# Kernel tuning notes

Measured on AMD Instinct MI355X. Metric: run time of the kernel, lower is better.

## Reference

```python
import jax, jax.numpy as jnp
import numpy as np

N_NODES = 100000
N_EDGES = 3200000
IN_CH = 16
HIDDEN = 32
NUM_HH = 1000


def setup_inputs() -> dict:
    key = jax.random.key(0)
    ks = jax.random.split(key, 10)
    x = jax.random.normal(ks[0], (N_NODES, IN_CH), dtype=jnp.float32)
    edge_index = jax.random.randint(ks[1], (2, N_EDGES), 0, N_NODES, dtype=jnp.int64)
    s = 1.0 / np.sqrt(IN_CH)
    w1_l = jax.random.uniform(ks[2], (IN_CH, HIDDEN), jnp.float32, -s, s)
    w1_r = jax.random.uniform(ks[3], (IN_CH, HIDDEN), jnp.float32, -s, s)
    b1 = jnp.zeros((HIDDEN,), jnp.float32)
    s2 = 1.0 / np.sqrt(HIDDEN)
    w2_l = jax.random.uniform(ks[4], (HIDDEN, HIDDEN), jnp.float32, -s2, s2)
    w2_r = jax.random.uniform(ks[5], (HIDDEN, HIDDEN), jnp.float32, -s2, s2)
    b2 = jnp.zeros((HIDDEN,), jnp.float32)
    fc_w = jax.random.uniform(ks[6], (HIDDEN, NUM_HH), jnp.float32, -s2, s2)
    fc_b = jnp.zeros((NUM_HH,), jnp.float32)
    return {"x": x, "edge_index": edge_index, "w1_l": w1_l, "w1_r": w1_r, "b1": b1,
            "w2_l": w2_l, "w2_r": w2_r, "b2": b2, "fc_w": fc_w, "fc_b": fc_b}


def _sage_conv(h, src, dst, w_l, w_r, b, n_nodes):
    # mean-aggregate source features onto targets (PyG SAGEConv, aggr='mean')
    msg = h[src]                                            # [E, F] gather
    agg = jax.ops.segment_sum(msg, dst, num_segments=n_nodes)
    cnt = jax.ops.segment_sum(jnp.ones((src.shape[0], 1), h.dtype), dst,
                              num_segments=n_nodes)
    mean = agg / jnp.maximum(cnt, 1.0)
    # out = lin_l(mean_neighbors) + lin_r(x); bias lives in lin_l
    return mean @ w_l + b + h @ w_r


def reference(x, edge_index, w1_l, w1_r, b1, w2_l, w2_r, b2, fc_w, fc_b):
    src, dst = edge_index[0], edge_index[1]
    n = x.shape[0]
    h = jax.nn.relu(_sage_conv(x, src, dst, w1_l, w1_r, b1, n))
    h = jax.nn.relu(_sage_conv(h, src, dst, w2_l, w2_r, b2, n))
    return h @ fc_w + fc_b
```

## Files before the change

kernel.cpp:

```cpp
#include <hip/hip_runtime.h>

#define N_NODES 100000
#define IN_CH 16
#define HIDDEN 32
#define NUM_HH 1000

#define NPB 128
#define NBUCK ((N_NODES + NPB - 1) / NPB)
#define NCHUNK 512
#define SCAN_N (NBUCK * NCHUNK)
#define S1_BLOCKS ((SCAN_N + 1023) / 1024)
#define SORT_CAP 6144

__global__ __launch_bounds__(256) void passA_count(const int* __restrict__ dst,
                                                   int* __restrict__ counts,
                                                   int n_edges, int cepb) {
  __shared__ int hist[NBUCK];
  for (int i = threadIdx.x; i < NBUCK; i += 256) hist[i] = 0;
  __syncthreads();
  const int s = blockIdx.x * cepb;
  const int e = min(n_edges, s + cepb);
  for (int i = s + threadIdx.x; i < e; i += 256)
    atomicAdd(&hist[dst[i] >> 7], 1);
  __syncthreads();
  for (int i = threadIdx.x; i < NBUCK; i += 256)
    counts[i * NCHUNK + blockIdx.x] = hist[i];
}

__global__ __launch_bounds__(1024) void scan_local(const int* __restrict__ in,
                                                   int* __restrict__ out,
                                                   int* __restrict__ partials) {
  __shared__ int tmp[1024];
  const int i = blockIdx.x * 1024 + threadIdx.x;
  const int v = (i < SCAN_N) ? in[i] : 0;
  tmp[threadIdx.x] = v;
  __syncthreads();
  for (int off = 1; off < 1024; off <<= 1) {
    int t = (threadIdx.x >= off) ? tmp[threadIdx.x - off] : 0;
    __syncthreads();
    tmp[threadIdx.x] += t;
    __syncthreads();
  }
  if (i < SCAN_N) out[i] = tmp[threadIdx.x] - v;
  if (threadIdx.x == 1023) partials[blockIdx.x] = tmp[threadIdx.x];
}

__global__ __launch_bounds__(512) void scan_partials(int* __restrict__ partials) {
  __shared__ int tmp[512];
  const int v = (threadIdx.x < S1_BLOCKS) ? partials[threadIdx.x] : 0;
  tmp[threadIdx.x] = v;
  __syncthreads();
  for (int off = 1; off < 512; off <<= 1) {
    int t = (threadIdx.x >= off) ? tmp[threadIdx.x - off] : 0;
    __syncthreads();
    tmp[threadIdx.x] += t;
    __syncthreads();
  }
  if (threadIdx.x < S1_BLOCKS) partials[threadIdx.x] = tmp[threadIdx.x] - v;
}

__global__ __launch_bounds__(1024) void scan_add(int* __restrict__ out,
                                                 const int* __restrict__ partials,
                                                 int* __restrict__ bucket_ptr,
                                                 int n_edges) {
  const int i = blockIdx.x * 1024 + threadIdx.x;
  if (i < SCAN_N) {
    const int v = out[i] + partials[blockIdx.x];
    out[i] = v;
    if ((i & (NCHUNK - 1)) == 0) bucket_ptr[i / NCHUNK] = v;
  }
  if (i == 0) bucket_ptr[NBUCK] = n_edges;
}

__global__ __launch_bounds__(256) void passB_scatter(
    const int* __restrict__ src, const int* __restrict__ dst,
    const int* __restrict__ offs, unsigned* __restrict__ packed, int n_edges,
    int cepb) {
  __shared__ int cur[NBUCK];
  for (int i = threadIdx.x; i < NBUCK; i += 256)
    cur[i] = offs[i * NCHUNK + blockIdx.x];
  __syncthreads();
  const int s = blockIdx.x * cepb;
  const int e = min(n_edges, s + cepb);
  for (int i = s + threadIdx.x; i < e; i += 256) {
    const int d = dst[i];
    const int b = d >> 7;
    const int pos = atomicAdd(&cur[b], 1);
    packed[pos] = (unsigned)src[i] | ((unsigned)(d & (NPB - 1)) << 17);
  }
}

__global__ __launch_bounds__(512) void bucket_sort(
    unsigned* __restrict__ packed, const int* __restrict__ bucket_ptr,
    int* __restrict__ row_ptr, int n_edges) {
  __shared__ unsigned stage[SORT_CAP];
  __shared__ int bins[NPB];
  __shared__ int scn[NPB];
  __shared__ int cur[NPB];
  const int b = blockIdx.x;
  const int s = bucket_ptr[b];
  const int cnt = bucket_ptr[b + 1] - s;
  const int tid = threadIdx.x;

  if (tid < NPB) bins[tid] = 0;
  __syncthreads();
  for (int i = tid; i < cnt; i += 512) {
    const unsigned pk = packed[s + i];
    stage[i] = pk;
    atomicAdd(&bins[pk >> 17], 1);
  }
  __syncthreads();
  if (tid < NPB) scn[tid] = bins[tid];
  __syncthreads();
  for (int off = 1; off < NPB; off <<= 1) {
    int t = (tid < NPB && tid >= off) ? scn[tid - off] : 0;
    __syncthreads();
    if (tid < NPB) scn[tid] += t;
    __syncthreads();
  }
  if (tid < NPB) {
    const int excl = scn[tid] - bins[tid];
    cur[tid] = excl;
    const int node = b * NPB + tid;
    if (node < N_NODES) row_ptr[node] = s + excl;
  }
  if (b == NBUCK - 1 && tid == 0) row_ptr[N_NODES] = n_edges;
  __syncthreads();
  for (int i = tid; i < cnt; i += 512) {
    const unsigned pk = stage[i];
    const int pos = atomicAdd(&cur[pk >> 17], 1);
    packed[s + pos] = pk & 0x1FFFFu;
  }
}

template <int CH, bool FC>
__global__ __launch_bounds__(512) void sage_block(
    const float* __restrict__ feat, const int* __restrict__ row_ptr,
    const int* __restrict__ adj, const float* __restrict__ w_l,
    const float* __restrict__ w_r, const float* __restrict__ b,
    float* __restrict__ out, const float* __restrict__ fcw,
    const float* __restrict__ fcb) {
  constexpr int Q = CH / 4;
  constexpr int EPW = 64 / Q;
  __shared__ float wl[CH * HIDDEN];
  __shared__ float wr[CH * HIDDEN];
  __shared__ float bs[HIDDEN];
  __shared__ float mean_s[8][CH];
  __shared__ float xs[8][CH];
  __shared__ float hs[FC ? NPB * HIDDEN : 1];

  const int tid = threadIdx.x;
  for (int i = tid; i < CH * HIDDEN; i += 512) {
    wl[i] = w_l[i];
    wr[i] = w_r[i];
  }
  if (tid < HIDDEN) bs[tid] = b[tid];
  __syncthreads();

  const int wave = tid >> 6;
  const int lane = tid & 63;
  const int base = blockIdx.x * NPB;
  const int q = lane & (Q - 1);
  const int esub = lane / Q;
  const int j = lane & 31;
  const int p = lane >> 5;

#pragma unroll 1
  for (int pass = 0; pass < NPB / 8; ++pass) {
    const int l = pass * 8 + wave;
    const int n = base + l;
    if (n < N_NODES) {
      const int s = row_ptr[n];
      const int e = row_ptr[n + 1];

      float4 acc = {0.f, 0.f, 0.f, 0.f};
      for (int i = s + esub; i < e; i += EPW) {
        const float4 v = ((const float4*)(feat + (size_t)adj[i] * CH))[q];
        acc.x += v.x;
        acc.y += v.y;
        acc.z += v.z;
        acc.w += v.w;
      }
#pragma unroll
      for (int m = Q; m < 64; m <<= 1) {
        acc.x += __shfl_xor(acc.x, m, 64);
        acc.y += __shfl_xor(acc.y, m, 64);
        acc.z += __shfl_xor(acc.z, m, 64);
        acc.w += __shfl_xor(acc.w, m, 64);
      }
      const float inv = 1.0f / fmaxf((float)(e - s), 1.0f);
      if (esub == 0) {
        mean_s[wave][4 * q + 0] = acc.x * inv;
        mean_s[wave][4 * q + 1] = acc.y * inv;
        mean_s[wave][4 * q + 2] = acc.z * inv;
        mean_s[wave][4 * q + 3] = acc.w * inv;
        const float4 xv = ((const float4*)(feat + (size_t)n * CH))[q];
        xs[wave][4 * q + 0] = xv.x;
        xs[wave][4 * q + 1] = xv.y;
        xs[wave][4 * q + 2] = xv.z;
        xs[wave][4 * q + 3] = xv.w;
      }
      __builtin_amdgcn_wave_barrier();

      float o = 0.f;
#pragma unroll
      for (int k = p * (CH / 2); k < (p + 1) * (CH / 2); ++k)
        o = fmaf(mean_s[wave][k], wl[k * HIDDEN + j],
                 fmaf(xs[wave][k], wr[k * HIDDEN + j], o));
      o += __shfl_xor(o, 32, 64);
      o = fmaxf(o + bs[j], 0.f);
      if (p == 0) {
        if (FC)
          hs[l * HIDDEN + j] = o;
        else
          out[(size_t)n * HIDDEN + j] = o;
      }
      __builtin_amdgcn_wave_barrier();
    }
  }

  if (FC) {
    __syncthreads();
    const int nvalid = min(NPB, N_NODES - base);
#pragma unroll
    for (int c = 0; c < 2; ++c) {
      const int jj = c * 512 + tid;
      if (jj < NUM_HH) {
        float w[HIDDEN];
#pragma unroll
        for (int k = 0; k < HIDDEN; ++k) w[k] = fcw[k * NUM_HH + jj];
        const float bias = fcb[jj];
        for (int n = 0; n < nvalid; ++n) {
          float a = bias;
#pragma unroll
          for (int k = 0; k < HIDDEN; ++k)
            a = fmaf(hs[n * HIDDEN + k], w[k], a);
          out[(size_t)(base + n) * NUM_HH + jj] = a;
        }
      }
    }
  }
}

extern "C" void kernel_launch(void* const* d_in, const int* in_sizes, int n_in,
                              void* d_out, int out_size, void* d_ws,
                              size_t ws_size, hipStream_t stream) {
  const float* x = (const float*)d_in[0];
  const int* edge = (const int*)d_in[1];
  const float* w1_l = (const float*)d_in[2];
  const float* w1_r = (const float*)d_in[3];
  const float* b1 = (const float*)d_in[4];
  const float* w2_l = (const float*)d_in[5];
  const float* w2_r = (const float*)d_in[6];
  const float* b2 = (const float*)d_in[7];
  const float* fc_w = (const float*)d_in[8];
  const float* fc_b = (const float*)d_in[9];
  float* out = (float*)d_out;

  const int n_edges = in_sizes[1] / 2;
  const int* src = edge;
  const int* dst = edge + n_edges;

  unsigned* packed = (unsigned*)d_ws;
  float* h1 = (float*)(packed + n_edges);
  int* counts = (int*)(h1 + (size_t)N_NODES * HIDDEN);
  int* offs = counts + SCAN_N;
  int* bucket_ptr = offs + SCAN_N;
  int* partials = bucket_ptr + NBUCK + 1;
  int* row_ptr = partials + S1_BLOCKS + 1;

  const int cepb = (n_edges + NCHUNK - 1) / NCHUNK;

  passA_count<<<NCHUNK, 256, 0, stream>>>(dst, counts, n_edges, cepb);
  scan_local<<<S1_BLOCKS, 1024, 0, stream>>>(counts, offs, partials);
  scan_partials<<<1, 512, 0, stream>>>(partials);
  scan_add<<<S1_BLOCKS, 1024, 0, stream>>>(offs, partials, bucket_ptr, n_edges);
  passB_scatter<<<NCHUNK, 256, 0, stream>>>(src, dst, offs, packed, n_edges,
                                            cepb);
  bucket_sort<<<NBUCK, 512, 0, stream>>>(packed, bucket_ptr, row_ptr, n_edges);

  sage_block<IN_CH, false><<<NBUCK, 512, 0, stream>>>(
      x, row_ptr, (const int*)packed, w1_l, w1_r, b1, h1, nullptr, nullptr);
  sage_block<HIDDEN, true><<<NBUCK, 512, 0, stream>>>(
      h1, row_ptr, (const int*)packed, w2_l, w2_r, b2, out, fc_w, fc_b);
}
```

Baseline: 459.5 us.

## Split final FC out of layer-2 SAGE kernel into register-tiled GEMM kernel

The fused FC epilogue in the second SAGE kernel is moved into a separate fc_reg kernel. Layer 2 now writes its hidden output to a new h2 workspace buffer. Each fc_reg thread keeps 4 output columns of the FC weights in registers and computes 4 outputs per node from shared-memory hidden rows. This is meant to raise FC throughput, since the old epilogue ran 512-thread blocks with one column and heavy serial loops per thread. The cost is an extra launch, a 12.8 MB round trip for h2, and higher register pressure.

```diff
diff --git a/kernel.cpp b/kernel.cpp
--- a/kernel.cpp
+++ b/kernel.cpp
@@ -133,13 +133,12 @@
   }
 }
 
-template <int CH, bool FC>
+template <int CH>
 __global__ __launch_bounds__(512) void sage_block(
     const float* __restrict__ feat, const int* __restrict__ row_ptr,
     const int* __restrict__ adj, const float* __restrict__ w_l,
     const float* __restrict__ w_r, const float* __restrict__ b,
-    float* __restrict__ out, const float* __restrict__ fcw,
-    const float* __restrict__ fcb) {
+    float* __restrict__ out) {
   constexpr int Q = CH / 4;
   constexpr int EPW = 64 / Q;
   __shared__ float wl[CH * HIDDEN];
@@ -147,7 +146,6 @@
   __shared__ float bs[HIDDEN];
   __shared__ float mean_s[8][CH];
   __shared__ float xs[8][CH];
-  __shared__ float hs[FC ? NPB * HIDDEN : 1];
 
   const int tid = threadIdx.x;
   for (int i = tid; i < CH * HIDDEN; i += 512) {
@@ -208,37 +206,67 @@
         o = fmaf(mean_s[wave][k], wl[k * HIDDEN + j],
                  fmaf(xs[wave][k], wr[k * HIDDEN + j], o));
       o += __shfl_xor(o, 32, 64);
-      o = fmaxf(o + bs[j], 0.f);
-      if (p == 0) {
-        if (FC)
-          hs[l * HIDDEN + j] = o;
-        else
-          out[(size_t)n * HIDDEN + j] = o;
-      }
+      if (p == 0) out[(size_t)n * HIDDEN + j] = fmaxf(o + bs[j], 0.f);
       __builtin_amdgcn_wave_barrier();
     }
   }
-
-  if (FC) {
-    __syncthreads();
-    const int nvalid = min(NPB, N_NODES - base);
-#pragma unroll
-    for (int c = 0; c < 2; ++c) {
-      const int jj = c * 512 + tid;
-      if (jj < NUM_HH) {
-        float w[HIDDEN];
-#pragma unroll
-        for (int k = 0; k < HIDDEN; ++k) w[k] = fcw[k * NUM_HH + jj];
-        const float bias = fcb[jj];
-        for (int n = 0; n < nvalid; ++n) {
-          float a = bias;
-#pragma unroll
-          for (int k = 0; k < HIDDEN; ++k)
-            a = fmaf(hs[n * HIDDEN + k], w[k], a);
-          out[(size_t)(base + n) * NUM_HH + jj] = a;
-        }
-      }
+}
+
+#define FC_BN 128
+__global__ __launch_bounds__(256) void fc_reg(
+    const float* __restrict__ h, const float* __restrict__ fcw,
+    const float* __restrict__ fcb, float* __restrict__ out) {
+  __shared__ float hs[FC_BN * HIDDEN];
+  const int tid = threadIdx.x;
+  const int base = blockIdx.x * FC_BN;
+  const int nvalid = min(FC_BN, N_NODES - base);
+
+  float w[4][HIDDEN];
+  float bias[4];
+#pragma unroll
+  for (int c = 0; c < 4; ++c) {
+    const int j = c * 256 + tid;
+    const bool valid = j < NUM_HH;
+    bias[c] = valid ? fcb[j] : 0.f;
+#pragma unroll
+    for (int k = 0; k < HIDDEN; ++k)
+      w[c][k] = valid ? fcw[k * NUM_HH + j] : 0.f;
+  }
+
+  const float4* s4 = (const float4*)(h + (size_t)base * HIDDEN);
+  for (int i = tid; i < nvalid * (HIDDEN / 4); i += 256)
+    ((float4*)hs)[i] = s4[i];
+  __syncthreads();
+
+#pragma unroll 2
+  for (int n = 0; n < nvalid; ++n) {
+    float a0 = bias[0], a1 = bias[1], a2 = bias[2], a3 = bias[3];
+    const float4* hrow = (const float4*)(hs + n * HIDDEN);
+#pragma unroll
+    for (int k4 = 0; k4 < HIDDEN / 4; ++k4) {
+      const float4 hv = hrow[k4];
+      a0 = fmaf(hv.x, w[0][4 * k4 + 0], a0);
+      a0 = fmaf(hv.y, w[0][4 * k4 + 1], a0);
+      a0 = fmaf(hv.z, w[0][4 * k4 + 2], a0);
+      a0 = fmaf(hv.w, w[0][4 * k4 + 3], a0);
+      a1 = fmaf(hv.x, w[1][4 * k4 + 0], a1);
+      a1 = fmaf(hv.y, w[1][4 * k4 + 1], a1);
+      a1 = fmaf(hv.z, w[1][4 * k4 + 2], a1);
+      a1 = fmaf(hv.w, w[1][4 * k4 + 3], a1);
+      a2 = fmaf(hv.x, w[2][4 * k4 + 0], a2);
+      a2 = fmaf(hv.y, w[2][4 * k4 + 1], a2);
+      a2 = fmaf(hv.z, w[2][4 * k4 + 2], a2);
+      a2 = fmaf(hv.w, w[2][4 * k4 + 3], a2);
+      a3 = fmaf(hv.x, w[3][4 * k4 + 0], a3);
+      a3 = fmaf(hv.y, w[3][4 * k4 + 1], a3);
+      a3 = fmaf(hv.z, w[3][4 * k4 + 2], a3);
+      a3 = fmaf(hv.w, w[3][4 * k4 + 3], a3);
     }
+    float* orow = out + (size_t)(base + n) * NUM_HH;
+    orow[tid] = a0;
+    orow[256 + tid] = a1;
+    orow[512 + tid] = a2;
+    if (768 + tid < NUM_HH) orow[768 + tid] = a3;
   }
 }
 
@@ -263,13 +291,15 @@
 
   unsigned* packed = (unsigned*)d_ws;
   float* h1 = (float*)(packed + n_edges);
-  int* counts = (int*)(h1 + (size_t)N_NODES * HIDDEN);
+  float* h2 = h1 + (size_t)N_NODES * HIDDEN;
+  int* counts = (int*)h2;
   int* offs = counts + SCAN_N;
-  int* bucket_ptr = offs + SCAN_N;
+  int* bucket_ptr = (int*)(h2 + (size_t)N_NODES * HIDDEN);
   int* partials = bucket_ptr + NBUCK + 1;
   int* row_ptr = partials + S1_BLOCKS + 1;
 
   const int cepb = (n_edges + NCHUNK - 1) / NCHUNK;
+  const int fgrid = (N_NODES + FC_BN - 1) / FC_BN;
 
   passA_count<<<NCHUNK, 256, 0, stream>>>(dst, counts, n_edges, cepb);
   scan_local<<<S1_BLOCKS, 1024, 0, stream>>>(counts, offs, partials);
@@ -279,8 +309,9 @@
                                             cepb);
   bucket_sort<<<NBUCK, 512, 0, stream>>>(packed, bucket_ptr, row_ptr, n_edges);
 
-  sage_block<IN_CH, false><<<NBUCK, 512, 0, stream>>>(
-      x, row_ptr, (const int*)packed, w1_l, w1_r, b1, h1, nullptr, nullptr);
-  sage_block<HIDDEN, true><<<NBUCK, 512, 0, stream>>>(
-      h1, row_ptr, (const int*)packed, w2_l, w2_r, b2, out, fc_w, fc_b);
-}
+  sage_block<IN_CH><<<NBUCK, 512, 0, stream>>>(x, row_ptr, (const int*)packed,
+                                               w1_l, w1_r, b1, h1);
+  sage_block<HIDDEN><<<NBUCK, 512, 0, stream>>>(h1, row_ptr, (const int*)packed,
+                                                w2_l, w2_r, b2, h2);
+  fc_reg<<<fgrid, 256, 0, stream>>>(h2, fc_w, fc_b, out);
+}
```

Measured after the change: 487.8 us. +6.2%, slower.
